# Kernel optimization log

Measured on AMD Instinct MI355X. Metric: run time of the kernel, lower is better.

The kernel has to match this reference:

```python
import jax, jax.numpy as jnp
import numpy as np

B, A, N, G, F = 16, 256, 64, 64, 128  # batch, atoms, neighbors, gaussians, filters
CUTOFF = 5.0


def ssp(x):
    # shifted softplus: ln(0.5*e^x + 0.5)
    return jax.nn.softplus(x) - jnp.log(2.0).astype(x.dtype)


def setup_inputs() -> dict:
    key = jax.random.key(0)
    ks = jax.random.split(key, 10)
    x = jax.random.normal(ks[0], (B, A, F), jnp.float32)
    r_ij = jax.random.uniform(ks[1], (B, A, N), jnp.float32) * 6.0  # some beyond cutoff
    f_ij = jax.random.uniform(ks[2], (B, A, N, G), jnp.float32)  # gaussian-expanded dists
    neighbors = jax.random.randint(ks[3], (B, A, N), 0, A)
    pairwise_mask = (jax.random.uniform(ks[4], (B, A, N)) < 0.9).astype(jnp.float32)
    s = lambda fan: 1.0 / np.sqrt(fan)
    fw1 = jax.random.normal(ks[5], (G, F), jnp.float32) * s(G)
    fb1 = jnp.zeros((F,), jnp.float32)
    fw2 = jax.random.normal(ks[6], (F, F), jnp.float32) * s(F)
    fb2 = jnp.zeros((F,), jnp.float32)
    w_in2f = jax.random.normal(ks[7], (F, F), jnp.float32) * s(F)
    w_f2out = jax.random.normal(ks[8], (F, F), jnp.float32) * s(F)
    b_f2out = jnp.zeros((F,), jnp.float32)
    return {"x": x, "r_ij": r_ij, "f_ij": f_ij, "neighbors": neighbors,
            "pairwise_mask": pairwise_mask, "fw1": fw1, "fb1": fb1, "fw2": fw2,
            "fb2": fb2, "w_in2f": w_in2f, "w_f2out": w_f2out, "b_f2out": b_f2out}


def reference(x, r_ij, f_ij, neighbors, pairwise_mask,
              fw1, fb1, fw2, fb2, w_in2f, w_f2out, b_f2out):
    # filter network: Dense(G->F, ssp) -> Dense(F->F)
    W = ssp(jnp.einsum('bang,gf->banf', f_ij, fw1) + fb1)
    W = jnp.einsum('banf,fh->banh', W, fw2) + fb2  # [B,A,N,F]
    # cosine cutoff
    C = 0.5 * (jnp.cos(r_ij * (jnp.pi / CUTOFF)) + 1.0)
    C = C * (r_ij < CUTOFF).astype(r_ij.dtype)
    W = W * C[..., None]
    # in2f (no bias), then gather neighbor features along atom axis
    y = jnp.einsum('bad,df->baf', x, w_in2f)  # [B,A,F]
    bidx = jnp.arange(y.shape[0])[:, None, None]
    y_nbh = y[bidx, neighbors]  # [B,A,N,F]
    # filter-weight multiply + masked sum aggregate over neighbor axis
    y = jnp.sum(y_nbh * W * pairwise_mask[..., None], axis=2)  # [B,A,F]
    # f2out with shifted-softplus activation
    return ssp(jnp.einsum('baf,fo->bao', y, w_f2out) + b_f2out)
```

## Files before the change

### kernel.cpp

```cpp
#include <hip/hip_runtime.h>
#include <hip/hip_bf16.h>
#include <math.h>

#define B_ 16
#define A_ 256
#define N_ 64
#define G_ 64
#define F_ 128

typedef __attribute__((ext_vector_type(8))) short short8;
typedef __attribute__((ext_vector_type(4))) float floatx4;

__device__ __forceinline__ float ssp(float x) {
    const float t = __expf(-fabsf(x));
    return fmaxf(x, 0.0f) + __logf(1.0f + t) - 0.69314718055994531f;
}
__device__ __forceinline__ unsigned f2bf(float f) {
    union { float f; unsigned u; } v; v.f = f;
    v.u += 0x7fffu + ((v.u >> 16) & 1u);
    return v.u >> 16;
}
__device__ __forceinline__ float bf2f_lo(unsigned d) {
    union { unsigned i; float f; } v; v.i = d << 16; return v.f;
}
__device__ __forceinline__ float bf2f_hi(unsigned d) {
    union { unsigned i; float f; } v; v.i = d & 0xffff0000u; return v.f;
}

__global__ __launch_bounds__(256) void k1_prep_in2f(
    const float* __restrict__ x,   const float* __restrict__ win,
    const float* __restrict__ fw1, const float* __restrict__ fw2,
    const float* __restrict__ wout,
    unsigned short* __restrict__ ypre,
    unsigned short* __restrict__ fw1B, unsigned short* __restrict__ fw2B,
    unsigned short* __restrict__ woutB)
{
    const int bid = blockIdx.x;
    const int tid = threadIdx.x;

    if (bid >= 256) {
        int idx = (bid - 256) * 1024 + tid * 4;
        #pragma unroll
        for (int u = 0; u < 4; ++u, ++idx) {
            if (idx < 8192) {
                const int j  = idx & 7;
                const int l  = (idx >> 3) & 63;
                const int ks = (idx >> 9) & 1;
                const int tf = idx >> 10;
                const int g  = ks * 32 + (l >> 4) * 8 + j;
                const int f  = tf * 16 + (l & 15);
                fw1B[idx] = (unsigned short)f2bf(fw1[g * F_ + f]);
            } else {
                const int i2 = (idx - 8192) & 16383;
                const int sel = (idx - 8192) >> 14;
                const int j  = i2 & 7;
                const int l  = (i2 >> 3) & 63;
                const int ks = (i2 >> 9) & 3;
                const int tf = i2 >> 11;
                const int k  = ks * 32 + (l >> 4) * 8 + j;
                const int f  = tf * 16 + (l & 15);
                if (sel == 0) fw2B[i2]  = (unsigned short)f2bf(fw2[k * F_ + f]);
                else          woutB[i2] = (unsigned short)f2bf(wout[k * F_ + f]);
            }
        }
        return;
    }

    __shared__ unsigned short s_wt[128 * 136];

    const float4* win4 = (const float4*)win;
    for (int i = tid; i < 4096; i += 256) {
        const float4 v = win4[i];
        const int e = i * 4;
        const int k = e >> 7;
        const int f = e & 127;
        s_wt[(f + 0) * 136 + k] = (unsigned short)f2bf(v.x);
        s_wt[(f + 1) * 136 + k] = (unsigned short)f2bf(v.y);
        s_wt[(f + 2) * 136 + k] = (unsigned short)f2bf(v.z);
        s_wt[(f + 3) * 136 + k] = (unsigned short)f2bf(v.w);
    }
    __syncthreads();

    const int w = tid >> 6, l = tid & 63, quad = l >> 4, c0 = l & 15;
    const int row0 = bid * 16;

    short8 a[4];
    {
        const float* base = x + (size_t)(row0 + c0) * F_ + quad * 8;
        #pragma unroll
        for (int ks = 0; ks < 4; ++ks) {
            const float4 v0 = *(const float4*)(base + ks * 32);
            const float4 v1 = *(const float4*)(base + ks * 32 + 4);
            short8 t;
            t[0] = (short)f2bf(v0.x); t[1] = (short)f2bf(v0.y);
            t[2] = (short)f2bf(v0.z); t[3] = (short)f2bf(v0.w);
            t[4] = (short)f2bf(v1.x); t[5] = (short)f2bf(v1.y);
            t[6] = (short)f2bf(v1.z); t[7] = (short)f2bf(v1.w);
            a[ks] = t;
        }
    }

    floatx4 acc[2];
    acc[0] = (floatx4){0.f,0.f,0.f,0.f};
    acc[1] = (floatx4){0.f,0.f,0.f,0.f};
    #pragma unroll
    for (int t = 0; t < 2; ++t) {
        const int tf = w * 2 + t;
        #pragma unroll
        for (int ks = 0; ks < 4; ++ks) {
            const short8 bfrag = *(const short8*)
                &s_wt[(tf * 16 + c0) * 136 + ks * 32 + quad * 8];
            acc[t] = __builtin_amdgcn_mfma_f32_16x16x32_bf16(
                a[ks], bfrag, acc[t], 0, 0, 0);
        }
    }
    #pragma unroll
    for (int r = 0; r < 4; ++r) {
        const int ro = row0 + quad * 4 + r;
        const unsigned lo = f2bf(acc[0][r]);
        const unsigned hi = f2bf(acc[1][r]);
        *(unsigned*)&ypre[(size_t)ro * F_ + c0 * 8 + w * 2] = lo | (hi << 16);
    }
}

__global__ __launch_bounds__(256) void cfconv_kernel(
    const float* __restrict__ r_ij, const float* __restrict__ f_ij,
    const int*   __restrict__ nbrs, const float* __restrict__ mask,
    const float* __restrict__ fb1,  const float* __restrict__ fb2,
    const unsigned short* __restrict__ ypre,
    const unsigned short* __restrict__ fw1B,
    const unsigned short* __restrict__ fw2B,
    unsigned short* __restrict__ y_agg)
{
    __shared__ short s_h1[N_ * F_];
    __shared__ float s_scale[N_];
    __shared__ int   s_nb[N_];
    __shared__ float s_red[4][F_];

    const int blk  = blockIdx.x;
    const int tid  = threadIdx.x;
    const int b    = blk >> 8;
    const int w    = tid >> 6;
    const int l    = tid & 63;
    const int quad = l >> 4;
    const int c0   = l & 15;

    if (l < 16) {
        const int n = w * 16 + l;
        const float r = r_ij[(size_t)blk * N_ + n];
        const float c = (r < 5.0f)
            ? 0.5f * (__cosf(r * 0.62831853071795865f) + 1.0f)
            : 0.0f;
        s_scale[n] = c * mask[(size_t)blk * N_ + n];
        s_nb[n]    = nbrs[(size_t)blk * N_ + n];
    }

    const short8* fw1B8 = (const short8*)fw1B;
    const short8* fw2B8 = (const short8*)fw2B;

    short8 a1[2];
    {
        const float* base = f_ij + (size_t)blk * (N_ * G_)
                          + (size_t)(w * 16 + c0) * G_ + quad * 8;
        #pragma unroll
        for (int ks = 0; ks < 2; ++ks) {
            const float4 v0 = *(const float4*)(base + ks * 32);
            const float4 v1 = *(const float4*)(base + ks * 32 + 4);
            short8 a;
            a[0] = (short)f2bf(v0.x); a[1] = (short)f2bf(v0.y);
            a[2] = (short)f2bf(v0.z); a[3] = (short)f2bf(v0.w);
            a[4] = (short)f2bf(v1.x); a[5] = (short)f2bf(v1.y);
            a[6] = (short)f2bf(v1.z); a[7] = (short)f2bf(v1.w);
            a1[ks] = a;
        }
    }
    floatx4 acc1[8];
    #pragma unroll
    for (int tf = 0; tf < 8; ++tf) acc1[tf] = (floatx4){0.f,0.f,0.f,0.f};
    #pragma unroll
    for (int ks = 0; ks < 2; ++ks)
        #pragma unroll
        for (int tf = 0; tf < 8; ++tf)
            acc1[tf] = __builtin_amdgcn_mfma_f32_16x16x32_bf16(
                a1[ks], fw1B8[(tf * 2 + ks) * 64 + l], acc1[tf], 0, 0, 0);

    #pragma unroll
    for (int tf = 0; tf < 8; ++tf) {
        const float bias  = fb1[tf * 16 + c0];
        const int   chunk = tf * 2 + (c0 >> 3);
        const int   o     = c0 & 7;
        #pragma unroll
        for (int r = 0; r < 4; ++r) {
            const int row_l = quad * 4 + r;
            const float v = ssp(acc1[tf][r] + bias);
            s_h1[(w * 16 + row_l) * F_ + ((chunk ^ row_l) * 8) + o] =
                (short)f2bf(v);
        }
    }

    short8 a2[4];
    #pragma unroll
    for (int ks = 0; ks < 4; ++ks)
        a2[ks] = *(const short8*)&s_h1[(w * 16 + c0) * F_
                                       + (((ks * 4 + quad) ^ c0) * 8)];

    float scl[4];
    uint4 yv[4];
    #pragma unroll
    for (int r = 0; r < 4; ++r) {
        const int n = w * 16 + quad * 4 + r;
        scl[r] = s_scale[n];
        yv[r] = *(const uint4*)&ypre[(size_t)(b * A_ + s_nb[n]) * F_ + c0 * 8];
    }

    floatx4 acc2[8];
    #pragma unroll
    for (int tf = 0; tf < 8; ++tf) acc2[tf] = (floatx4){0.f,0.f,0.f,0.f};
    #pragma unroll
    for (int ks = 0; ks < 4; ++ks)
        #pragma unroll
        for (int tf = 0; tf < 8; ++tf)
            acc2[tf] = __builtin_amdgcn_mfma_f32_16x16x32_bf16(
                a2[ks], fw2B8[(tf * 4 + ks) * 64 + l], acc2[tf], 0, 0, 0);

    float part[8];
    #pragma unroll
    for (int tf = 0; tf < 8; ++tf) part[tf] = 0.0f;
    #pragma unroll
    for (int r = 0; r < 4; ++r) {
        const unsigned d0 = yv[r].x, d1 = yv[r].y, d2 = yv[r].z, d3 = yv[r].w;
        part[0] = fmaf((acc2[0][r] + fb2[0*16+c0]) * scl[r], bf2f_lo(d0), part[0]);
        part[1] = fmaf((acc2[1][r] + fb2[1*16+c0]) * scl[r], bf2f_hi(d0), part[1]);
        part[2] = fmaf((acc2[2][r] + fb2[2*16+c0]) * scl[r], bf2f_lo(d1), part[2]);
        part[3] = fmaf((acc2[3][r] + fb2[3*16+c0]) * scl[r], bf2f_hi(d1), part[3]);
        part[4] = fmaf((acc2[4][r] + fb2[4*16+c0]) * scl[r], bf2f_lo(d2), part[4]);
        part[5] = fmaf((acc2[5][r] + fb2[5*16+c0]) * scl[r], bf2f_hi(d2), part[5]);
        part[6] = fmaf((acc2[6][r] + fb2[6*16+c0]) * scl[r], bf2f_lo(d3), part[6]);
        part[7] = fmaf((acc2[7][r] + fb2[7*16+c0]) * scl[r], bf2f_hi(d3), part[7]);
    }

    #pragma unroll
    for (int tf = 0; tf < 8; ++tf) {
        part[tf] += __shfl_xor(part[tf], 16, 64);
        part[tf] += __shfl_xor(part[tf], 32, 64);
    }
    if (l < 16) {
        #pragma unroll
        for (int tf = 0; tf < 8; ++tf)
            s_red[w][tf * 16 + l] = part[tf];
    }
    __syncthreads();

    if (tid < F_) {
        const float v = s_red[0][tid] + s_red[1][tid]
                      + s_red[2][tid] + s_red[3][tid];
        y_agg[(size_t)blk * F_ + tid] = (unsigned short)f2bf(v);
    }
}

__global__ __launch_bounds__(256) void f2out_kernel(
    const unsigned short* __restrict__ y_agg,
    const unsigned short* __restrict__ woutB,
    const float* __restrict__ bias, float* __restrict__ out)
{
    const int tid = threadIdx.x;
    const int w = tid >> 6, l = tid & 63, quad = l >> 4, c0 = l & 15;
    const int row = blockIdx.x * 64 + w * 16 + c0;

    short8 a[4];
    #pragma unroll
    for (int ks = 0; ks < 4; ++ks)
        a[ks] = *(const short8*)&y_agg[(size_t)row * F_ + ks * 32 + quad * 8];

    const short8* W8 = (const short8*)woutB;
    floatx4 acc[8];
    #pragma unroll
    for (int tf = 0; tf < 8; ++tf) acc[tf] = (floatx4){0.f,0.f,0.f,0.f};
    #pragma unroll
    for (int ks = 0; ks < 4; ++ks)
        #pragma unroll
        for (int tf = 0; tf < 8; ++tf)
            acc[tf] = __builtin_amdgcn_mfma_f32_16x16x32_bf16(
                a[ks], W8[(tf * 4 + ks) * 64 + l], acc[tf], 0, 0, 0);

    #pragma unroll
    for (int tf = 0; tf < 8; ++tf) {
        const float bs = bias[tf * 16 + c0];
        #pragma unroll
        for (int r = 0; r < 4; ++r) {
            const int ro = blockIdx.x * 64 + w * 16 + quad * 4 + r;
            out[(size_t)ro * F_ + tf * 16 + c0] = ssp(acc[tf][r] + bs);
        }
    }
}

extern "C" void kernel_launch(void* const* d_in, const int* in_sizes, int n_in,
                              void* d_out, int out_size, void* d_ws, size_t ws_size,
                              hipStream_t stream) {
    const float* x        = (const float*)d_in[0];
    const float* r_ij     = (const float*)d_in[1];
    const float* f_ij     = (const float*)d_in[2];
    const int*   nbrs     = (const int*)  d_in[3];
    const float* mask     = (const float*)d_in[4];
    const float* fw1      = (const float*)d_in[5];
    const float* fb1      = (const float*)d_in[6];
    const float* fw2      = (const float*)d_in[7];
    const float* fb2      = (const float*)d_in[8];
    const float* w_in2f   = (const float*)d_in[9];
    const float* w_f2out  = (const float*)d_in[10];
    const float* b_f2out  = (const float*)d_in[11];
    float* out = (float*)d_out;

    unsigned short* ypre  = (unsigned short*)d_ws;
    unsigned short* fw1B  = ypre  + (size_t)B_ * A_ * F_;
    unsigned short* fw2B  = fw1B  + 8192;
    unsigned short* woutB = fw2B  + 16384;
    unsigned short* y_agg = woutB + 16384;

    k1_prep_in2f<<<296, 256, 0, stream>>>(
        x, w_in2f, fw1, fw2, w_f2out, ypre, fw1B, fw2B, woutB);
    cfconv_kernel<<<B_ * A_, 256, 0, stream>>>(
        r_ij, f_ij, nbrs, mask, fb1, fb2, ypre, fw1B, fw2B, y_agg);
    f2out_kernel<<<B_ * A_ / 64, 256, 0, stream>>>(y_agg, woutB, b_f2out, out);
}
```

Before: 164.1 us.

## Split cfconv filter columns across 8 waves and separate weight repack from in2f GEMM

The cfconv kernel now runs 512 threads per block, with two wave groups each computing half of the 128 filter columns for the same 16 neighbor rows. This halves per-wave MFMA work and accumulator registers, which should raise occupancy and latency hiding. The cost is redundant f_ij loads and a block barrier before the shared h1 tile is read. Separately, all weight repacking (including w_in2f) moves into its own small kernel, and the in2f GEMM reads pre-packed fragments instead of transposing w_in2f through shared memory in every block. That adds one more kernel launch.

```diff
diff --git a/kernel.cpp b/kernel.cpp
--- a/kernel.cpp
+++ b/kernel.cpp
@@ -27,66 +27,52 @@
     union { unsigned i; float f; } v; v.i = d & 0xffff0000u; return v.f;
 }
 
-__global__ __launch_bounds__(256) void k1_prep_in2f(
-    const float* __restrict__ x,   const float* __restrict__ win,
+__global__ __launch_bounds__(256) void k0_repack(
     const float* __restrict__ fw1, const float* __restrict__ fw2,
-    const float* __restrict__ wout,
-    unsigned short* __restrict__ ypre,
+    const float* __restrict__ win, const float* __restrict__ wout,
     unsigned short* __restrict__ fw1B, unsigned short* __restrict__ fw2B,
-    unsigned short* __restrict__ woutB)
+    unsigned short* __restrict__ winB, unsigned short* __restrict__ woutB)
 {
-    const int bid = blockIdx.x;
+    int idx = blockIdx.x * 1024 + threadIdx.x * 4;
+    #pragma unroll
+    for (int u = 0; u < 4; ++u, ++idx) {
+        if (idx < 8192) {
+            const int j  = idx & 7;
+            const int l  = (idx >> 3) & 63;
+            const int ks = (idx >> 9) & 1;
+            const int tf = idx >> 10;
+            const int g  = ks * 32 + (l >> 4) * 8 + j;
+            const int f  = tf * 16 + (l & 15);
+            fw1B[idx] = (unsigned short)f2bf(fw1[g * F_ + f]);
+        } else {
+            const int i2  = (idx - 8192) & 16383;
+            const int sel = (idx - 8192) >> 14;
+            const int j  = i2 & 7;
+            const int l  = (i2 >> 3) & 63;
+            const int ks = (i2 >> 9) & 3;
+            const int tf = i2 >> 11;
+            const int k  = ks * 32 + (l >> 4) * 8 + j;
+            const int f  = tf * 16 + (l & 15);
+            const float v = (sel == 0) ? fw2[k * F_ + f]
+                          : (sel == 1) ? win[k * F_ + f]
+                                       : wout[k * F_ + f];
+            unsigned short* dst = (sel == 0) ? fw2B : (sel == 1) ? winB : woutB;
+            dst[i2] = (unsigned short)f2bf(v);
+        }
+    }
+}
+
+__global__ __launch_bounds__(256) void in2f_gemm(
+    const float* __restrict__ x, const unsigned short* __restrict__ winB,
+    unsigned short* __restrict__ ypre)
+{
     const int tid = threadIdx.x;
-
-    if (bid >= 256) {
-        int idx = (bid - 256) * 1024 + tid * 4;
-        #pragma unroll
-        for (int u = 0; u < 4; ++u, ++idx) {
-            if (idx < 8192) {
-                const int j  = idx & 7;
-                const int l  = (idx >> 3) & 63;
-                const int ks = (idx >> 9) & 1;
-                const int tf = idx >> 10;
-                const int g  = ks * 32 + (l >> 4) * 8 + j;
-                const int f  = tf * 16 + (l & 15);
-                fw1B[idx] = (unsigned short)f2bf(fw1[g * F_ + f]);
-            } else {
-                const int i2 = (idx - 8192) & 16383;
-                const int sel = (idx - 8192) >> 14;
-                const int j  = i2 & 7;
-                const int l  = (i2 >> 3) & 63;
-                const int ks = (i2 >> 9) & 3;
-                const int tf = i2 >> 11;
-                const int k  = ks * 32 + (l >> 4) * 8 + j;
-                const int f  = tf * 16 + (l & 15);
-                if (sel == 0) fw2B[i2]  = (unsigned short)f2bf(fw2[k * F_ + f]);
-                else          woutB[i2] = (unsigned short)f2bf(wout[k * F_ + f]);
-            }
-        }
-        return;
-    }
-
-    __shared__ unsigned short s_wt[128 * 136];
-
-    const float4* win4 = (const float4*)win;
-    for (int i = tid; i < 4096; i += 256) {
-        const float4 v = win4[i];
-        const int e = i * 4;
-        const int k = e >> 7;
-        const int f = e & 127;
-        s_wt[(f + 0) * 136 + k] = (unsigned short)f2bf(v.x);
-        s_wt[(f + 1) * 136 + k] = (unsigned short)f2bf(v.y);
-        s_wt[(f + 2) * 136 + k] = (unsigned short)f2bf(v.z);
-        s_wt[(f + 3) * 136 + k] = (unsigned short)f2bf(v.w);
-    }
-    __syncthreads();
-
     const int w = tid >> 6, l = tid & 63, quad = l >> 4, c0 = l & 15;
-    const int row0 = bid * 16;
+    const int row = blockIdx.x * 64 + w * 16 + c0;
 
     short8 a[4];
     {
-        const float* base = x + (size_t)(row0 + c0) * F_ + quad * 8;
+        const float* base = x + (size_t)row * F_ + quad * 8;
         #pragma unroll
         for (int ks = 0; ks < 4; ++ks) {
             const float4 v0 = *(const float4*)(base + ks * 32);
@@ -100,30 +86,28 @@
         }
     }
 
-    floatx4 acc[2];
-    acc[0] = (floatx4){0.f,0.f,0.f,0.f};
-    acc[1] = (floatx4){0.f,0.f,0.f,0.f};
-    #pragma unroll
-    for (int t = 0; t < 2; ++t) {
-        const int tf = w * 2 + t;
-        #pragma unroll
-        for (int ks = 0; ks < 4; ++ks) {
-            const short8 bfrag = *(const short8*)
-                &s_wt[(tf * 16 + c0) * 136 + ks * 32 + quad * 8];
-            acc[t] = __builtin_amdgcn_mfma_f32_16x16x32_bf16(
-                a[ks], bfrag, acc[t], 0, 0, 0);
-        }
-    }
+    const short8* W8 = (const short8*)winB;
+    floatx4 acc[8];
+    #pragma unroll
+    for (int tf = 0; tf < 8; ++tf) acc[tf] = (floatx4){0.f,0.f,0.f,0.f};
+    #pragma unroll
+    for (int ks = 0; ks < 4; ++ks)
+        #pragma unroll
+        for (int tf = 0; tf < 8; ++tf)
+            acc[tf] = __builtin_amdgcn_mfma_f32_16x16x32_bf16(
+                a[ks], W8[(tf * 4 + ks) * 64 + l], acc[tf], 0, 0, 0);
+
     #pragma unroll
     for (int r = 0; r < 4; ++r) {
-        const int ro = row0 + quad * 4 + r;
-        const unsigned lo = f2bf(acc[0][r]);
-        const unsigned hi = f2bf(acc[1][r]);
-        *(unsigned*)&ypre[(size_t)ro * F_ + c0 * 8 + w * 2] = lo | (hi << 16);
-    }
-}
-
-__global__ __launch_bounds__(256) void cfconv_kernel(
+        const int ro = blockIdx.x * 64 + w * 16 + quad * 4 + r;
+        short8 s;
+        #pragma unroll
+        for (int tf = 0; tf < 8; ++tf) s[tf] = (short)f2bf(acc[tf][r]);
+        *(short8*)&ypre[(size_t)ro * F_ + c0 * 8] = s;
+    }
+}
+
+__global__ __launch_bounds__(512, 5) void cfconv_kernel(
     const float* __restrict__ r_ij, const float* __restrict__ f_ij,
     const int*   __restrict__ nbrs, const float* __restrict__ mask,
     const float* __restrict__ fb1,  const float* __restrict__ fb2,
@@ -144,9 +128,11 @@
     const int l    = tid & 63;
     const int quad = l >> 4;
     const int c0   = l & 15;
-
-    if (l < 16) {
-        const int n = w * 16 + l;
+    const int rw   = w & 3;
+    const int h    = w >> 2;
+
+    if (h == 0 && l < 16) {
+        const int n = rw * 16 + l;
         const float r = r_ij[(size_t)blk * N_ + n];
         const float c = (r < 5.0f)
             ? 0.5f * (__cosf(r * 0.62831853071795865f) + 1.0f)
@@ -161,7 +147,7 @@
     short8 a1[2];
     {
         const float* base = f_ij + (size_t)blk * (N_ * G_)
-                          + (size_t)(w * 16 + c0) * G_ + quad * 8;
+                          + (size_t)(rw * 16 + c0) * G_ + quad * 8;
         #pragma unroll
         for (int ks = 0; ks < 2; ++ks) {
             const float4 v0 = *(const float4*)(base + ks * 32);
@@ -174,80 +160,83 @@
             a1[ks] = a;
         }
     }
-    floatx4 acc1[8];
-    #pragma unroll
-    for (int tf = 0; tf < 8; ++tf) acc1[tf] = (floatx4){0.f,0.f,0.f,0.f};
+    floatx4 acc1[4];
+    #pragma unroll
+    for (int t = 0; t < 4; ++t) acc1[t] = (floatx4){0.f,0.f,0.f,0.f};
     #pragma unroll
     for (int ks = 0; ks < 2; ++ks)
         #pragma unroll
-        for (int tf = 0; tf < 8; ++tf)
-            acc1[tf] = __builtin_amdgcn_mfma_f32_16x16x32_bf16(
-                a1[ks], fw1B8[(tf * 2 + ks) * 64 + l], acc1[tf], 0, 0, 0);
-
-    #pragma unroll
-    for (int tf = 0; tf < 8; ++tf) {
+        for (int t = 0; t < 4; ++t) {
+            const int tf = h * 4 + t;
+            acc1[t] = __builtin_amdgcn_mfma_f32_16x16x32_bf16(
+                a1[ks], fw1B8[(tf * 2 + ks) * 64 + l], acc1[t], 0, 0, 0);
+        }
+
+    #pragma unroll
+    for (int t = 0; t < 4; ++t) {
+        const int   tf    = h * 4 + t;
         const float bias  = fb1[tf * 16 + c0];
         const int   chunk = tf * 2 + (c0 >> 3);
         const int   o     = c0 & 7;
         #pragma unroll
         for (int r = 0; r < 4; ++r) {
             const int row_l = quad * 4 + r;
-            const float v = ssp(acc1[tf][r] + bias);
-            s_h1[(w * 16 + row_l) * F_ + ((chunk ^ row_l) * 8) + o] =
+            const float v = ssp(acc1[t][r] + bias);
+            s_h1[(rw * 16 + row_l) * F_ + ((chunk ^ row_l) * 8) + o] =
                 (short)f2bf(v);
         }
     }
+    __syncthreads();
 
     short8 a2[4];
     #pragma unroll
     for (int ks = 0; ks < 4; ++ks)
-        a2[ks] = *(const short8*)&s_h1[(w * 16 + c0) * F_
+        a2[ks] = *(const short8*)&s_h1[(rw * 16 + c0) * F_
                                        + (((ks * 4 + quad) ^ c0) * 8)];
 
     float scl[4];
-    uint4 yv[4];
+    uint2 yv[4];
     #pragma unroll
     for (int r = 0; r < 4; ++r) {
-        const int n = w * 16 + quad * 4 + r;
+        const int n = rw * 16 + quad * 4 + r;
         scl[r] = s_scale[n];
-        yv[r] = *(const uint4*)&ypre[(size_t)(b * A_ + s_nb[n]) * F_ + c0 * 8];
-    }
-
-    floatx4 acc2[8];
-    #pragma unroll
-    for (int tf = 0; tf < 8; ++tf) acc2[tf] = (floatx4){0.f,0.f,0.f,0.f};
-    #pragma unroll
-    for (int ks = 0; ks < 4; ++ks)
-        #pragma unroll
-        for (int tf = 0; tf < 8; ++tf)
-            acc2[tf] = __builtin_amdgcn_mfma_f32_16x16x32_bf16(
-                a2[ks], fw2B8[(tf * 4 + ks) * 64 + l], acc2[tf], 0, 0, 0);
-
-    float part[8];
-    #pragma unroll
-    for (int tf = 0; tf < 8; ++tf) part[tf] = 0.0f;
+        yv[r] = *(const uint2*)&ypre[(size_t)(b * A_ + s_nb[n]) * F_
+                                     + c0 * 8 + h * 4];
+    }
+
+    floatx4 acc2[4];
+    #pragma unroll
+    for (int t = 0; t < 4; ++t) acc2[t] = (floatx4){0.f,0.f,0.f,0.f};
+    #pragma unroll
+    for (int ks = 0; ks < 4; ++ks)
+        #pragma unroll
+        for (int t = 0; t < 4; ++t) {
+            const int tf = h * 4 + t;
+            acc2[t] = __builtin_amdgcn_mfma_f32_16x16x32_bf16(
+                a2[ks], fw2B8[(tf * 4 + ks) * 64 + l], acc2[t], 0, 0, 0);
+        }
+
+    float part[4];
+    #pragma unroll
+    for (int t = 0; t < 4; ++t) part[t] = 0.0f;
     #pragma unroll
     for (int r = 0; r < 4; ++r) {
-        const unsigned d0 = yv[r].x, d1 = yv[r].y, d2 = yv[r].z, d3 = yv[r].w;
-        part[0] = fmaf((acc2[0][r] + fb2[0*16+c0]) * scl[r], bf2f_lo(d0), part[0]);
-        part[1] = fmaf((acc2[1][r] + fb2[1*16+c0]) * scl[r], bf2f_hi(d0), part[1]);
-        part[2] = fmaf((acc2[2][r] + fb2[2*16+c0]) * scl[r], bf2f_lo(d1), part[2]);
-        part[3] = fmaf((acc2[3][r] + fb2[3*16+c0]) * scl[r], bf2f_hi(d1), part[3]);
-        part[4] = fmaf((acc2[4][r] + fb2[4*16+c0]) * scl[r], bf2f_lo(d2), part[4]);
-        part[5] = fmaf((acc2[5][r] + fb2[5*16+c0]) * scl[r], bf2f_hi(d2), part[5]);
-        part[6] = fmaf((acc2[6][r] + fb2[6*16+c0]) * scl[r], bf2f_lo(d3), part[6]);
-        part[7] = fmaf((acc2[7][r] + fb2[7*16+c0]) * scl[r], bf2f_hi(d3), part[7]);
-    }
-
-    #pragma unroll
-    for (int tf = 0; tf < 8; ++tf) {
-        part[tf] += __shfl_xor(part[tf], 16, 64);
-        part[tf] += __shfl_xor(part[tf], 32, 64);
+        const unsigned d0 = yv[r].x, d1 = yv[r].y;
+        part[0] = fmaf((acc2[0][r] + fb2[(h*4+0)*16+c0]) * scl[r], bf2f_lo(d0), part[0]);
+        part[1] = fmaf((acc2[1][r] + fb2[(h*4+1)*16+c0]) * scl[r], bf2f_hi(d0), part[1]);
+        part[2] = fmaf((acc2[2][r] + fb2[(h*4+2)*16+c0]) * scl[r], bf2f_lo(d1), part[2]);
+        part[3] = fmaf((acc2[3][r] + fb2[(h*4+3)*16+c0]) * scl[r], bf2f_hi(d1), part[3]);
+    }
+
+    #pragma unroll
+    for (int t = 0; t < 4; ++t) {
+        part[t] += __shfl_xor(part[t], 16, 64);
+        part[t] += __shfl_xor(part[t], 32, 64);
     }
     if (l < 16) {
         #pragma unroll
-        for (int tf = 0; tf < 8; ++tf)
-            s_red[w][tf * 16 + l] = part[tf];
+        for (int t = 0; t < 4; ++t)
+            s_red[rw][(h * 4 + t) * 16 + l] = part[t];
     }
     __syncthreads();
 
@@ -314,12 +303,14 @@
     unsigned short* ypre  = (unsigned short*)d_ws;
     unsigned short* fw1B  = ypre  + (size_t)B_ * A_ * F_;
     unsigned short* fw2B  = fw1B  + 8192;
-    unsigned short* woutB = fw2B  + 16384;
+    unsigned short* winB  = fw2B  + 16384;
+    unsigned short* woutB = winB  + 16384;
     unsigned short* y_agg = woutB + 16384;
 
-    k1_prep_in2f<<<296, 256, 0, stream>>>(
-        x, w_in2f, fw1, fw2, w_f2out, ypre, fw1B, fw2B, woutB);
-    cfconv_kernel<<<B_ * A_, 256, 0, stream>>>(
+    k0_repack<<<56, 256, 0, stream>>>(
+        fw1, fw2, w_in2f, w_f2out, fw1B, fw2B, winB, woutB);
+    in2f_gemm<<<B_ * A_ / 64, 256, 0, stream>>>(x, winB, ypre);
+    cfconv_kernel<<<B_ * A_, 512, 0, stream>>>(
         r_ij, f_ij, nbrs, mask, fb1, fb2, ypre, fw1B, fw2B, y_agg);
     f2out_kernel<<<B_ * A_ / 64, 256, 0, stream>>>(y_agg, woutB, b_f2out, out);
 }
```

Result: no change. 166.5 us (+1.5%).
